# Kernel optimization log

Measured on AMD Instinct MI355X. Metric: run time of the kernel, lower is better.

## Reference

```python
import jax, jax.numpy as jnp
import numpy as np

D, H, L, FF, V, B, S = 512, 8, 6, 2048, 4096, 2, 4096
EPS = 1e-5

def _unit(v):
    return v / jnp.linalg.norm(v, axis=-1, keepdims=True)

def _unitelu(v):
    return jax.nn.elu(_unit(v))

def _ln(x, g, b):
    m = jnp.mean(x, axis=-1, keepdims=True)
    var = jnp.var(x, axis=-1, keepdims=True)
    return (x - m) * jax.lax.rsqrt(var + EPS) * g + b

def setup_inputs() -> dict:
    key = jax.random.key(0)
    ks = jax.random.split(key, 16)
    s = 0.02
    inp = {
        'input': jax.random.randint(ks[0], (B, S), 0, V),
        'emb': jax.random.normal(ks[1], (V, D)) * s,
        'Wq': jax.random.normal(ks[2], (L, D, D)) * s,
        'bq': jnp.zeros((L, D)),
        'Wk': jax.random.normal(ks[3], (L, D, D)) * s,
        'bk': jnp.zeros((L, D)),
        'Wv': jax.random.normal(ks[4], (L, D, D)) * s,
        'bv': jnp.zeros((L, D)),
        'Wo': jax.random.normal(ks[5], (L, D, D)) * s,
        'bo': jnp.zeros((L, D)),
        'W1': jax.random.normal(ks[6], (L, FF, D)) * s,
        'b1': jnp.zeros((L, FF)),
        'W2': jax.random.normal(ks[7], (L, D, FF)) * s,
        'b2': jnp.zeros((L, D)),
        'g2': jnp.ones((L, D)),
        'be2': jnp.zeros((L, D)),
        'Wfc': jax.random.normal(ks[8], (V, D)) * s,
        'bfc': jnp.zeros((V,)),
    }
    return inp

def reference(input, emb, Wq, bq, Wk, bk, Wv, bv, Wo, bo, W1, b1, W2, b2, g2, be2, Wfc, bfc):
    # h: [S, B, D] (seq-major, matching input.permute(1,0) then embedding)
    h = emb[input.T]
    for l in range(L):
        # linear kernelized attention: O(S * dh^2) per head, no SxS matrix
        k = _unitelu((h @ Wk[l].T + bk[l]).reshape(S, B, H, -1))  # [S,B,H,dh]
        v = (h @ Wv[l].T + bv[l]).reshape(S, B, H, -1)
        A = jnp.einsum('sbnq,sbnv->bnvq', k, v)                    # [B,H,dh,dh]
        q = _unit((h @ Wq[l].T + bq[l]).reshape(S, B, H, -1))
        o = jnp.einsum('sbnq,bnvq->sbnv', q, A).reshape(S, B, D)
        h = h + (o @ Wo[l].T + bo[l])
        f = jax.nn.relu(h @ W1[l].T + b1[l]) @ W2[l].T + b2[l]
        h = _ln(h + f, g2[l], be2[l])
    out = h @ Wfc.T + bfc          # [S, B, V]
    return out.transpose(1, 2, 0)  # [B, V, S]
```

## Files before the change

kernel.cpp:

```cpp
#include <hip/hip_runtime.h>
#include <hip/hip_bf16.h>

#define D_  512
#define H_  8
#define DH_ 64
#define L_  6
#define FF_ 2048
#define V_  4096
#define B_  2
#define S_  4096
#define SB_ (S_*B_)
#define DD_ ((size_t)D_*D_)
#define FD_ ((size_t)FF_*D_)
#define NTOT_ (4*DD_ + 2*FD_)
#define CVT_BLKS_ 20480

typedef unsigned short u16;
typedef unsigned int   u32;
typedef _Float16 f16;
typedef f16   f16x8 __attribute__((ext_vector_type(8)));
typedef float f32x4 __attribute__((ext_vector_type(4)));

__device__ __forceinline__ float us2f(u16 u){
  union { u32 i; float f; } c; c.i = ((u32)u) << 16; return c.f;
}
__device__ __forceinline__ u16 f2b(float f){
  union { float f; u32 i; } c; c.f = f;
  u32 x = c.i;
  x += 0x7FFF + ((x >> 16) & 1);
  return (u16)(x >> 16);
}
__device__ __forceinline__ float h2f(u16 u){
  union { u16 s; f16 h; } c; c.s = u; return (float)c.h;
}
__device__ __forceinline__ u16 f2h(float f){
  union { f16 h; u16 s; } c; c.h = (f16)f; return c.s;
}
__device__ __forceinline__ float ldf(const void* p, size_t i, int isbf){
  return isbf ? us2f(((const u16*)p)[i]) : ((const float*)p)[i];
}

typedef const __attribute__((address_space(1))) u32* gas_u32p;
typedef       __attribute__((address_space(3))) u32* las_u32p;
__device__ __forceinline__ void async16(const u16* g, u16* l){
  __builtin_amdgcn_global_load_lds((gas_u32p)(const void*)g, (las_u32p)(void*)l, 16, 0, 0);
}

__global__ __launch_bounds__(64) void detect_dtype(const void* emb, int* flag)
{
  const int t = threadIdx.x;
  u16 hw = ((const u16*)emb)[t];
  int e = (hw >> 7) & 0xFF;
  int ok = ((e > 96) && (e < 160)) || ((hw & 0x7FFF) == 0);
  unsigned long long m = __ballot(ok);
  if (t == 0) *flag = (__popcll(m) >= 56) ? 1 : 0;
}

__global__ __launch_bounds__(256) void prep_all(
    const void* Wq, const void* Wk, const void* Wv, const void* Wo,
    const void* W1, const void* W2, const void* Wfc,
    u16* __restrict__ dstAll, u16* __restrict__ dstFC,
    const int* __restrict__ inp, const void* emb,
    float* __restrict__ h, u16* __restrict__ hb, const int* flagp)
{
  const int isbf = *flagp;
  if (blockIdx.x >= CVT_BLKS_) {
    const int m = blockIdx.x - CVT_BLKS_;
    const int t = threadIdx.x;
    const int s = m >> 1, b = m & 1;
    const int tok = inp[b * S_ + s];
    #pragma unroll
    for (int hh = 0; hh < 2; hh++) {
      const int d = t + hh * 256;
      const float v = ldf(emb, (size_t)tok * D_ + d, isbf);
      h[(size_t)m * D_ + d] = v;
      hb[(size_t)m * D_ + d] = f2h(v);
    }
    return;
  }
  const size_t total6 = 6 * NTOT_;
  const size_t i = ((size_t)blockIdx.x * 256 + threadIdx.x) * 4;
  const void* src; size_t off; u16* dst;
  if (i < total6) {
    const int l = (int)(i / NTOT_);
    const size_t r = i - (size_t)l * NTOT_;
    const size_t n4 = 4 * DD_, nW1 = n4 + FD_;
    if (r < n4) {
      const int wsel = (int)(r / DD_);
      src = (wsel == 0) ? Wq : (wsel == 1) ? Wk : (wsel == 2) ? Wv : Wo;
      off = (size_t)l * DD_ + (r - (size_t)wsel * DD_);
    } else if (r < nW1) { src = W1; off = (size_t)l * FD_ + (r - n4); }
    else                { src = W2; off = (size_t)l * FD_ + (r - nW1); }
    dst = dstAll + i;
  } else {
    const size_t j = i - total6;
    if (j >= (size_t)V_ * D_) return;
    src = Wfc; off = j; dst = dstFC + j;
  }
  ushort4 o;
  if (isbf) {
    ushort4 u = *(const ushort4*)((const u16*)src + off);
    o = make_ushort4(f2h(us2f(u.x)), f2h(us2f(u.y)), f2h(us2f(u.z)), f2h(us2f(u.w)));
  } else {
    float4 f = *(const float4*)((const float*)src + off);
    o = make_ushort4(f2h(f.x), f2h(f.y), f2h(f.z), f2h(f.w));
  }
  *(ushort4*)dst = o;
}

template<int ACT, int OUTMODE, int PRE, int TPB, int LOG_TX, int LOG_TXZ>
__global__ __launch_bounds__(256) void gemm_pers(
    const u16* __restrict__ A, const u16* __restrict__ Bm,
    int bstride,
    const void* bias, size_t bias_off,
    u16* __restrict__ Cb, void* __restrict__ Cout,
    int M, int N, int K, const int* flagp)
{
  __shared__ u16 tile[(PRE + 1) * 8192];
  const int t = threadIdx.x, lane = t & 63, w = t >> 6;
  const int wr = w >> 1, wc = w & 1;
  const int col = lane & 15, quad = lane >> 4;
  const int srow = w * 16 + (lane >> 2);
  const int skol = (((lane & 3) ^ ((lane >> 3) & 3)) << 3);
  const int rswz = ((col >> 1) & 3);
  const int isbf = *flagp;
  const int vbase = blockIdx.x * TPB;

  float bpre3[(OUTMODE == 3) ? 16 : 1];
  float bpre0[(OUTMODE == 3) ? 1 : TPB][4];
  if (OUTMODE == 3) {
    const int by0 = vbase >> LOG_TXZ;
    #pragma unroll
    for (int i = 0; i < 4; i++)
      #pragma unroll
      for (int r = 0; r < 4; r++)
        bpre3[i * 4 + r] = ldf(bias, bias_off + (by0 << 7) + wr * 64 + i * 16 + quad * 4 + r, isbf);
  } else {
    #pragma unroll
    for (int g = 0; g < TPB; g++) {
      const int bxg = (vbase + g) & ((1 << LOG_TX) - 1);
      #pragma unroll
      for (int j = 0; j < 4; j++)
        bpre0[g][j] = ldf(bias, bias_off + (bxg << 7) + wc * 64 + j * 16 + col, isbf);
    }
  }

  int st = -1;
  const u16 *ag0 = nullptr, *ag1 = nullptr, *bg0 = nullptr, *bg1 = nullptr;
  auto set_tile = [&](int tp) {
    const int v  = vbase + tp;
    const int by = v >> LOG_TXZ;
    const int rr = v & ((1 << LOG_TXZ) - 1);
    const int bz = rr >> LOG_TX;
    const int bx = rr & ((1 << LOG_TX) - 1);
    ag0 = A + (size_t)((by << 7) + srow) * K + skol;
    ag1 = ag0 + (size_t)64 * K;
    bg0 = Bm + ((size_t)((bx << 7) + srow) * bstride + bz) * K + skol;
    bg1 = bg0 + (size_t)64 * bstride * K;
  };
  auto stage = [&](int u) {
    const int tp = u >> 4;
    if (tp != st) { st = tp; set_tile(tp); }
    const int k0 = (u & 15) << 5;
    const int bo = (u % (PRE + 1)) * 8192;
    async16(ag0 + k0, &tile[bo +        w * 512]);
    async16(ag1 + k0, &tile[bo + 2048 + w * 512]);
    async16(bg0 + k0, &tile[bo + 4096 + w * 512]);
    async16(bg1 + k0, &tile[bo + 6144 + w * 512]);
  };

  const int U = TPB * 16;
  #pragma unroll
  for (int p = 0; p < PRE; ++p) stage(p);
  if (PRE >= 2) asm volatile("s_waitcnt vmcnt(4)" ::: "memory");
  else          asm volatile("s_waitcnt vmcnt(0)" ::: "memory");
  __builtin_amdgcn_s_barrier();
  asm volatile("" ::: "memory");

  f32x4 acc[4][4] = {};
  for (int u = 0; u < U; ++u) {
    if (u + PRE < U) stage(u + PRE);
    const int cur = (u % (PRE + 1)) * 8192;
    f16x8 af[4], bf[4];
    #pragma unroll
    for (int i = 0; i < 4; i++)
      af[i] = *(const f16x8*)&tile[cur + (wr * 64 + i * 16 + col) * 32 + ((quad ^ rswz) * 8)];
    #pragma unroll
    for (int j = 0; j < 4; j++)
      bf[j] = *(const f16x8*)&tile[cur + 4096 + (wc * 64 + j * 16 + col) * 32 + ((quad ^ rswz) * 8)];
    #pragma unroll
    for (int i = 0; i < 4; i++)
      #pragma unroll
      for (int j = 0; j < 4; j++)
        acc[i][j] = __builtin_amdgcn_mfma_f32_16x16x32_f16(af[i], bf[j], acc[i][j], 0, 0, 0);

    if ((u & 15) == 15) {
      const int v  = vbase + (u >> 4);
      const int by = v >> LOG_TXZ;
      const int rr = v & ((1 << LOG_TXZ) - 1);
      const int bz = rr >> LOG_TX;
      const int bx = rr & ((1 << LOG_TX) - 1);
      const int bm = by << 7, bn = bx << 7;
      if (OUTMODE == 3) {
        const size_t obase = (size_t)bz * M * N;
        #pragma unroll
        for (int i = 0; i < 4; i++)
          #pragma unroll
          for (int r = 0; r < 4; r++) {
            const int m = bm + wr * 64 + i * 16 + quad * 4 + r;
            #pragma unroll
            for (int j = 0; j < 4; j++) {
              const int n = bn + wc * 64 + j * 16 + col;
              const float c = acc[i][j][r] + bpre3[i * 4 + r];
              const size_t oi = obase + (size_t)m * N + n;
              if (isbf) ((u16*)Cout)[oi] = f2b(c);
              else      ((float*)Cout)[oi] = c;
            }
          }
      } else {
        const int g = u >> 4;
        #pragma unroll
        for (int i = 0; i < 4; i++)
          #pragma unroll
          for (int r = 0; r < 4; r++) {
            const int m = bm + wr * 64 + i * 16 + quad * 4 + r;
            #pragma unroll
            for (int j = 0; j < 4; j++) {
              const int n = bn + wc * 64 + j * 16 + col;
              float c = acc[i][j][r] + bpre0[g][j];
              if (ACT == 1) c = fmaxf(c, 0.f);
              Cb[(size_t)m * N + n] = f2h(c);
            }
          }
      }
      const f32x4 z = {0.f, 0.f, 0.f, 0.f};
      #pragma unroll
      for (int i = 0; i < 4; i++)
        #pragma unroll
        for (int j = 0; j < 4; j++)
          acc[i][j] = z;
    }

    if (PRE >= 2 && u + 2 < U) asm volatile("s_waitcnt vmcnt(4)" ::: "memory");
    else                       asm volatile("s_waitcnt vmcnt(0)" ::: "memory");
    __builtin_amdgcn_s_barrier();
    asm volatile("" ::: "memory");
  }
}

__global__ __launch_bounds__(256) void gemm_qkv(
    const u16* __restrict__ A, const u16* __restrict__ Bm,
    const void* bq, const void* bk, const void* bv, size_t b_off,
    u16* __restrict__ qb, u16* __restrict__ kb, u16* __restrict__ vb,
    int K, const int* flagp)
{
  __shared__ u16 tile[3 * 8192];
  const int t = threadIdx.x, lane = t & 63, w = t >> 6;
  const int bm = blockIdx.y << 7, bn = blockIdx.x << 7;
  const int wr = w >> 1, wc = w & 1;
  const int col = lane & 15, quad = lane >> 4;

  const int srow = w * 16 + (lane >> 2);
  const int skol = (((lane & 3) ^ ((lane >> 3) & 3)) << 3);
  const u16* ag0 = A + (size_t)(bm + srow) * K + skol;
  const u16* ag1 = A + (size_t)(bm + 64 + srow) * K + skol;
  const u16* bg0 = Bm + (size_t)(bn + srow) * K + skol;
  const u16* bg1 = Bm + (size_t)(bn + 64 + srow) * K + skol;
  u16* la0 = &tile[       w * 512];
  u16* la1 = &tile[2048 + w * 512];
  u16* lb0 = &tile[4096 + w * 512];
  u16* lb1 = &tile[6144 + w * 512];

  const int nt = K >> 5;

  #pragma unroll
  for (int p = 0; p < 2; ++p) {
    const int k0 = p << 5, bo = p * 8192;
    async16(ag0 + k0, la0 + bo);
    async16(ag1 + k0, la1 + bo);
    async16(bg0 + k0, lb0 + bo);
    async16(bg1 + k0, lb1 + bo);
  }
  asm volatile("s_waitcnt vmcnt(4)" ::: "memory");
  __builtin_amdgcn_s_barrier();
  asm volatile("" ::: "memory");

  const int rswz = ((col >> 1) & 3);

  f32x4 acc[4][4] = {};
  for (int t2 = 0; t2 < nt; ++t2) {
    if (t2 + 2 < nt) {
      const int k0 = (t2 + 2) << 5;
      const int bo = ((t2 + 2) % 3) * 8192;
      async16(ag0 + k0, la0 + bo);
      async16(ag1 + k0, la1 + bo);
      async16(bg0 + k0, lb0 + bo);
      async16(bg1 + k0, lb1 + bo);
    }
    const int cur = (t2 % 3) * 8192;
    f16x8 af[4], bf[4];
    #pragma unroll
    for (int i = 0; i < 4; i++)
      af[i] = *(const f16x8*)&tile[cur + (wr * 64 + i * 16 + col) * 32 + ((quad ^ rswz) * 8)];
    #pragma unroll
    for (int j = 0; j < 4; j++)
      bf[j] = *(const f16x8*)&tile[cur + 4096 + (wc * 64 + j * 16 + col) * 32 + ((quad ^ rswz) * 8)];
    #pragma unroll
    for (int i = 0; i < 4; i++)
      #pragma unroll
      for (int j = 0; j < 4; j++)
        acc[i][j] = __builtin_amdgcn_mfma_f32_16x16x32_f16(af[i], bf[j], acc[i][j], 0, 0, 0);
    if (t2 + 2 < nt) asm volatile("s_waitcnt vmcnt(4)" ::: "memory");
    else             asm volatile("s_waitcnt vmcnt(0)" ::: "memory");
    __builtin_amdgcn_s_barrier();
    asm volatile("" ::: "memory");
  }

  const int isbf = *flagp;
  const int nbase = bn + wc * 64;
  const int sel = nbase >> 9;
  const int nl0 = nbase & 511;
  u16* outp = (sel == 0) ? qb : (sel == 1) ? kb : vb;
  const void* bias = (sel == 0) ? bq : (sel == 1) ? bk : bv;

  if (sel < 2) {
    #pragma unroll
    for (int i = 0; i < 4; i++) {
      #pragma unroll
      for (int r = 0; r < 4; r++) {
        float v[4]; float ss = 0.f;
        #pragma unroll
        for (int j = 0; j < 4; j++) {
          const int nl = nl0 + j * 16 + col;
          v[j] = acc[i][j][r] + ldf(bias, b_off + nl, isbf);
          ss += v[j] * v[j];
        }
        ss += __shfl_xor(ss, 1); ss += __shfl_xor(ss, 2);
        ss += __shfl_xor(ss, 4); ss += __shfl_xor(ss, 8);
        const float inv = rsqrtf(fmaxf(ss, 1e-30f));
        const int m = bm + wr * 64 + i * 16 + quad * 4 + r;
        #pragma unroll
        for (int j = 0; j < 4; j++) {
          float u = v[j] * inv;
          if (sel == 1) u = (u > 0.f) ? u : expm1f(u);
          outp[(size_t)m * 512 + nl0 + j * 16 + col] = f2h(u);
        }
      }
    }
  } else {
    #pragma unroll
    for (int i = 0; i < 4; i++)
      #pragma unroll
      for (int r = 0; r < 4; r++) {
        const int m = bm + wr * 64 + i * 16 + quad * 4 + r;
        #pragma unroll
        for (int j = 0; j < 4; j++) {
          const int nl = nl0 + j * 16 + col;
          outp[(size_t)m * 512 + nl] = f2h(acc[i][j][r] + ldf(bias, b_off + nl, isbf));
        }
      }
  }
}

template<int ACT, int OUTMODE, int PRE>
__global__ __launch_bounds__(256) void gemm_mfma64(
    const u16* __restrict__ A, const u16* __restrict__ Bm,
    const void* bias, size_t bias_off,
    const float* __restrict__ res,
    float* __restrict__ Cf, u16* __restrict__ Cb,
    int M, int N, int K, const int* flagp)
{
  __shared__ u16 tile[(PRE + 1) * 6144];
  const int t = threadIdx.x, lane = t & 63, w = t >> 6;
  const int bm = blockIdx.y << 6, bn = blockIdx.x << 7;
  const int wr = w >> 1, wc = w & 1;
  const int col = lane & 15, quad = lane >> 4;

  const int srow = w * 16 + (lane >> 2);
  const int skol = (((lane & 3) ^ ((lane >> 3) & 3)) << 3);
  const u16* ag  = A + (size_t)(bm + srow) * K + skol;
  const u16* bg0 = Bm + (size_t)(bn + srow) * K + skol;
  const u16* bg1 = Bm + (size_t)(bn + 64 + srow) * K + skol;
  u16* la  = &tile[       w * 512];
  u16* lb0 = &tile[2048 + w * 512];
  u16* lb1 = &tile[4096 + w * 512];

  const int nt = K >> 5;

  #pragma unroll
  for (int p = 0; p < PRE; ++p) {
    const int k0 = p << 5, bo = p * 6144;
    async16(ag  + k0, la  + bo);
    async16(bg0 + k0, lb0 + bo);
    async16(bg1 + k0, lb1 + bo);
  }
  if      (PRE >= 3) asm volatile("s_waitcnt vmcnt(6)" ::: "memory");
  else if (PRE == 2) asm volatile("s_waitcnt vmcnt(3)" ::: "memory");
  else               asm volatile("s_waitcnt vmcnt(0)" ::: "memory");
  __builtin_amdgcn_s_barrier();
  asm volatile("" ::: "memory");

  const int rswz = ((col >> 1) & 3);

  f32x4 acc[2][4] = {};
  for (int t2 = 0; t2 < nt; ++t2) {
    if (t2 + PRE < nt) {
      const int k0 = (t2 + PRE) << 5;
      const int bo = ((t2 + PRE) % (PRE + 1)) * 6144;
      async16(ag  + k0, la  + bo);
      async16(bg0 + k0, lb0 + bo);
      async16(bg1 + k0, lb1 + bo);
    }
    const int cur = (t2 % (PRE + 1)) * 6144;
    f16x8 af[2], bf[4];
    #pragma unroll
    for (int i = 0; i < 2; i++)
      af[i] = *(const f16x8*)&tile[cur + (wr * 32 + i * 16 + col) * 32 + ((quad ^ rswz) * 8)];
    #pragma unroll
    for (int j = 0; j < 4; j++)
      bf[j] = *(const f16x8*)&tile[cur + 2048 + (wc * 64 + j * 16 + col) * 32 + ((quad ^ rswz) * 8)];
    #pragma unroll
    for (int i = 0; i < 2; i++)
      #pragma unroll
      for (int j = 0; j < 4; j++)
        acc[i][j] = __builtin_amdgcn_mfma_f32_16x16x32_f16(af[i], bf[j], acc[i][j], 0, 0, 0);
    if (PRE >= 3) {
      if      (t2 + 3 < nt) asm volatile("s_waitcnt vmcnt(6)" ::: "memory");
      else if (t2 + 2 < nt) asm volatile("s_waitcnt vmcnt(3)" ::: "memory");
      else                  asm volatile("s_waitcnt vmcnt(0)" ::: "memory");
    } else if (PRE == 2) {
      if (t2 + 2 < nt) asm volatile("s_waitcnt vmcnt(3)" ::: "memory");
      else             asm volatile("s_waitcnt vmcnt(0)" ::: "memory");
    } else {
      asm volatile("s_waitcnt vmcnt(0)" ::: "memory");
    }
    __builtin_amdgcn_s_barrier();
    asm volatile("" ::: "memory");
  }

  const int isbf = *flagp;
  #pragma unroll
  for (int i = 0; i < 2; i++) {
    #pragma unroll
    for (int r = 0; r < 4; r++) {
      const int m = bm + wr * 32 + i * 16 + quad * 4 + r;
      #pragma unroll
      for (int j = 0; j < 4; j++) {
        const int n = bn + wc * 64 + j * 16 + col;
        float c = acc[i][j][r] + ldf(bias, bias_off + n, isbf);
        if (res) c += res[(size_t)m * N + n];
        if (ACT == 1) c = fmaxf(c, 0.f);
        if (OUTMODE == 0) {
          Cb[(size_t)m * N + n] = f2h(c);
        } else if (OUTMODE == 1) {
          Cf[(size_t)m * N + n] = c;
          Cb[(size_t)m * N + n] = f2h(c);
        } else {
          Cf[(size_t)m * N + n] = c;
        }
      }
    }
  }
}

#define KT_ 136
__global__ __launch_bounds__(256) void attn_acc_mfma(
    const u16* __restrict__ kbuf, const u16* __restrict__ vbuf,
    float* __restrict__ Apart)
{
  __shared__ u16 ktr[64 * KT_];
  __shared__ u16 vtr[64 * KT_];
  const int bh = blockIdx.x;
  const int b  = bh >> 3, n = bh & 7;
  const int s0 = blockIdx.y << 7;
  const int t = threadIdx.x, lane = t & 63, w = t >> 6;
  const int col = lane & 15, quad = lane >> 4;

  #pragma unroll
  for (int u = 0; u < 8; u++) {
    const int flat = u * 256 + t;
    const int row = flat >> 4, q4 = (flat & 15) << 2;
    const size_t g = ((size_t)(s0 + row) * B_ + b) * D_ + n * 64 + q4;
    ushort4 kk = *(const ushort4*)&kbuf[g];
    ushort4 vv = *(const ushort4*)&vbuf[g];
    ktr[(q4+0)*KT_ + row] = kk.x; ktr[(q4+1)*KT_ + row] = kk.y;
    ktr[(q4+2)*KT_ + row] = kk.z; ktr[(q4+3)*KT_ + row] = kk.w;
    vtr[(q4+0)*KT_ + row] = vv.x; vtr[(q4+1)*KT_ + row] = vv.y;
    vtr[(q4+2)*KT_ + row] = vv.z; vtr[(q4+3)*KT_ + row] = vv.w;
  }
  __syncthreads();

  f32x4 acc[4] = {};
  #pragma unroll
  for (int ks = 0; ks < 4; ks++) {
    const int k0 = ks * 32;
    f16x8 af = *(const f16x8*)&vtr[(w * 16 + col) * KT_ + k0 + quad * 8];
    #pragma unroll
    for (int j = 0; j < 4; j++) {
      f16x8 bf = *(const f16x8*)&ktr[(j * 16 + col) * KT_ + k0 + quad * 8];
      acc[j] = __builtin_amdgcn_mfma_f32_16x16x32_f16(af, bf, acc[j], 0, 0, 0);
    }
  }
  float* Ap = Apart + ((size_t)blockIdx.y * 16 + bh) * 4096;
  #pragma unroll
  for (int j = 0; j < 4; j++)
    #pragma unroll
    for (int r = 0; r < 4; r++) {
      const int vi = w * 16 + quad * 4 + r, qi = j * 16 + col;
      Ap[vi * 64 + qi] = acc[j][r];
    }
}

__global__ __launch_bounds__(256) void reduce_A(
    const float* __restrict__ Apart, u16* __restrict__ Ah)
{
  const int i = blockIdx.x * 256 + threadIdx.x;
  const int bh = i >> 12, idx = i & 4095;
  float s = 0.f;
  #pragma unroll
  for (int p = 0; p < 32; p++)
    s += Apart[((size_t)p * 16 + bh) * 4096 + idx];
  Ah[i] = f2h(s);
}

__global__ __launch_bounds__(256) void attn_apply_mfma(
    u16* __restrict__ qo, const u16* __restrict__ Ah)
{
  const int bh = blockIdx.x;
  const int b = bh >> 3, n = bh & 7;
  const int s0 = blockIdx.y << 7;
  const int t = threadIdx.x, lane = t & 63, w = t >> 6;
  const int col = lane & 15, quad = lane >> 4;

  const u16* Ab_ = Ah + (size_t)bh * 4096;
  f16x8 bf[4][2];
  #pragma unroll
  for (int j = 0; j < 4; j++)
    #pragma unroll
    for (int ks = 0; ks < 2; ks++)
      bf[j][ks] = *(const f16x8*)&Ab_[(j * 16 + col) * 64 + ks * 32 + quad * 8];

  const int srow_base = s0 + w * 32;
  f32x4 acc[2][4] = {};
  #pragma unroll
  for (int i = 0; i < 2; i++) {
    const int s = srow_base + i * 16 + col;
    const u16* qp = qo + ((size_t)s * B_ + b) * D_ + n * 64;
    f16x8 af0 = *(const f16x8*)&qp[quad * 8];
    f16x8 af1 = *(const f16x8*)&qp[32 + quad * 8];
    #pragma unroll
    for (int j = 0; j < 4; j++) {
      acc[i][j] = __builtin_amdgcn_mfma_f32_16x16x32_f16(af0, bf[j][0], acc[i][j], 0, 0, 0);
      acc[i][j] = __builtin_amdgcn_mfma_f32_16x16x32_f16(af1, bf[j][1], acc[i][j], 0, 0, 0);
    }
  }
  #pragma unroll
  for (int i = 0; i < 2; i++)
    #pragma unroll
    for (int r = 0; r < 4; r++) {
      const int s = srow_base + i * 16 + quad * 4 + r;
      u16* op = qo + ((size_t)s * B_ + b) * D_ + n * 64;
      #pragma unroll
      for (int j = 0; j < 4; j++)
        op[j * 16 + col] = f2h(acc[i][j][r]);
    }
}

__global__ __launch_bounds__(256) void ln_k(
    float* __restrict__ h, u16* __restrict__ hb,
    const void* g, size_t g_off, const void* be, size_t be_off, const int* flagp)
{
  const int isbf = *flagp;
  const int m = blockIdx.x, t = threadIdx.x;
  float* p = h + (size_t)m * D_;
  const float x0 = p[t], x1 = p[t + 256];
  __shared__ float red[4];
  float s = x0 + x1;
  #pragma unroll
  for (int off = 32; off >= 1; off >>= 1) s += __shfl_xor(s, off);
  if ((t & 63) == 0) red[t >> 6] = s;
  __syncthreads();
  const float mean = (red[0] + red[1] + red[2] + red[3]) * (1.f / 512.f);
  const float d0 = x0 - mean, d1 = x1 - mean;
  float s2 = d0 * d0 + d1 * d1;
  #pragma unroll
  for (int off = 32; off >= 1; off >>= 1) s2 += __shfl_xor(s2, off);
  __syncthreads();
  if ((t & 63) == 0) red[t >> 6] = s2;
  __syncthreads();
  const float var = (red[0] + red[1] + red[2] + red[3]) * (1.f / 512.f);
  const float sc = rsqrtf(var + 1e-5f);
  const float y0 = d0 * sc * ldf(g, g_off + t, isbf)       + ldf(be, be_off + t, isbf);
  const float y1 = d1 * sc * ldf(g, g_off + t + 256, isbf) + ldf(be, be_off + t + 256, isbf);
  p[t] = y0;       p[t + 256] = y1;
  hb[(size_t)m * D_ + t] = f2h(y0);
  hb[(size_t)m * D_ + t + 256] = f2h(y1);
}

extern "C" void kernel_launch(void* const* d_in, const int* in_sizes, int n_in,
                              void* d_out, int out_size, void* d_ws, size_t ws_size,
                              hipStream_t stream) {
  const int*  inp = (const int*) d_in[0];
  const void* emb = d_in[1];
  const void* Wq  = d_in[2];
  const void* bq  = d_in[3];
  const void* Wk  = d_in[4];
  const void* bk  = d_in[5];
  const void* Wv  = d_in[6];
  const void* bv  = d_in[7];
  const void* Wo  = d_in[8];
  const void* bo  = d_in[9];
  const void* W1  = d_in[10];
  const void* b1  = d_in[11];
  const void* W2  = d_in[12];
  const void* b2  = d_in[13];
  const void* g2  = d_in[14];
  const void* be2 = d_in[15];
  const void* Wfc = d_in[16];
  const void* bfc = d_in[17];

  char* ws = (char*)d_ws;
  float* h     = (float*)(ws);
  u16*   hb    = (u16*)  (ws + 16777216);
  u16*   qb    = (u16*)  (ws + 25165824);
  u16*   kb    = (u16*)  (ws + 33554432);
  u16*   vb    = (u16*)  (ws + 41943040);
  u16*   mid   = qb;
  float* Apart = (float*)(ws + 58720256);
  u16*   Ah16  = (u16*)  (ws + 67108864);
  u16*   WcAll = (u16*)  (ws + 67239936);
  u16*   WcFC  = (u16*)  (ws + 104988672);
  int*   flag  = (int*)  (ws + 109182976);

  detect_dtype<<<1, 64, 0, stream>>>(emb, flag);
  prep_all<<<CVT_BLKS_ + SB_, 256, 0, stream>>>(
      Wq, Wk, Wv, Wo, W1, W2, Wfc, WcAll, WcFC, inp, emb, h, hb, flag);

  const dim3 gQ64(D_ / 128, SB_ / 64);
  const dim3 gQKV(3 * D_ / 128, SB_ / 128);
  const dim3 gAT(B_ * H_, S_ / 128);

  for (int l = 0; l < L_; l++) {
    u16* Wcl = WcAll + (size_t)l * NTOT_;

    gemm_qkv<<<gQKV, 256, 0, stream>>>(hb, Wcl, bq, bk, bv, (size_t)l*D_, qb, kb, vb, D_, flag);

    attn_acc_mfma<<<gAT, 256, 0, stream>>>(kb, vb, Apart);
    reduce_A<<<256, 256, 0, stream>>>(Apart, Ah16);
    attn_apply_mfma<<<gAT, 256, 0, stream>>>(qb, Ah16);

    gemm_mfma64<0,1,3><<<gQ64, 256, 0, stream>>>(qb, Wcl + 3*DD_, bo, (size_t)l*D_, h, h, hb, SB_, D_, D_, flag);
    gemm_pers<1,0,2,2,4,4><<<512, 256, 0, stream>>>(hb, Wcl + 4*DD_, 1, b1, (size_t)l*FF_, mid, nullptr, SB_, FF_, D_, flag);
    gemm_mfma64<0,2,3><<<gQ64, 256, 0, stream>>>(mid, Wcl + 4*DD_ + FD_, b2, (size_t)l*D_, h, h, nullptr, SB_, D_, FF_, flag);
    ln_k<<<SB_, 256, 0, stream>>>(h, hb, g2, (size_t)l*D_, be2, (size_t)l*D_, flag);
  }

  gemm_pers<0,3,2,4,5,6><<<512, 256, 0, stream>>>(WcFC, hb, 2, bfc, 0, nullptr, d_out, V_, S_, D_, flag);
}
```

Measured before the change: 1.337 ms.

## Fold attention state into per-batch Wo weights, removing the attention-apply pass

```diff
diff --git a/kernel.cpp b/kernel.cpp
--- a/kernel.cpp
+++ b/kernel.cpp
@@ -463,6 +463,87 @@
   }
 }
 
+__global__ __launch_bounds__(256) void gemm_wo(
+    const u16* __restrict__ A,
+    const u16* __restrict__ Wp,
+    const void* bias, size_t bias_off,
+    float* __restrict__ h, u16* __restrict__ hb, const int* flagp)
+{
+  __shared__ u16 tile[4 * 6144];
+  const int t = threadIdx.x, lane = t & 63, w = t >> 6;
+  const int bm = blockIdx.y << 6, bn = blockIdx.x << 7, bz = blockIdx.z;
+  const int wr = w >> 1, wc = w & 1;
+  const int col = lane & 15, quad = lane >> 4;
+
+  const int srow = w * 16 + (lane >> 2);
+  const int skol = (((lane & 3) ^ ((lane >> 3) & 3)) << 3);
+  const u16* ag  = A + ((size_t)(bm + srow) * 2 + bz) * 512 + skol;
+  const u16* bg0 = Wp + (size_t)bz * 512 * 512 + (size_t)(bn + srow) * 512 + skol;
+  const u16* bg1 = bg0 + (size_t)64 * 512;
+  u16* la  = &tile[       w * 512];
+  u16* lb0 = &tile[2048 + w * 512];
+  u16* lb1 = &tile[4096 + w * 512];
+
+  #pragma unroll
+  for (int p = 0; p < 3; ++p) {
+    const int k0 = p << 5, bo = p * 6144;
+    async16(ag  + k0, la  + bo);
+    async16(bg0 + k0, lb0 + bo);
+    async16(bg1 + k0, lb1 + bo);
+  }
+  asm volatile("s_waitcnt vmcnt(6)" ::: "memory");
+  __builtin_amdgcn_s_barrier();
+  asm volatile("" ::: "memory");
+
+  const int rswz = ((col >> 1) & 3);
+
+  f32x4 acc[2][4] = {};
+  for (int t2 = 0; t2 < 16; ++t2) {
+    if (t2 + 3 < 16) {
+      const int k0 = (t2 + 3) << 5;
+      const int bo = ((t2 + 3) & 3) * 6144;
+      async16(ag  + k0, la  + bo);
+      async16(bg0 + k0, lb0 + bo);
+      async16(bg1 + k0, lb1 + bo);
+    }
+    const int cur = (t2 & 3) * 6144;
+    f16x8 af[2], bf[4];
+    #pragma unroll
+    for (int i = 0; i < 2; i++)
+      af[i] = *(const f16x8*)&tile[cur + (wr * 32 + i * 16 + col) * 32 + ((quad ^ rswz) * 8)];
+    #pragma unroll
+    for (int j = 0; j < 4; j++)
+      bf[j] = *(const f16x8*)&tile[cur + 2048 + (wc * 64 + j * 16 + col) * 32 + ((quad ^ rswz) * 8)];
+    #pragma unroll
+    for (int i = 0; i < 2; i++)
+      #pragma unroll
+      for (int j = 0; j < 4; j++)
+        acc[i][j] = __builtin_amdgcn_mfma_f32_16x16x32_f16(af[i], bf[j], acc[i][j], 0, 0, 0);
+    if      (t2 + 3 < 16) asm volatile("s_waitcnt vmcnt(6)" ::: "memory");
+    else if (t2 + 2 < 16) asm volatile("s_waitcnt vmcnt(3)" ::: "memory");
+    else                  asm volatile("s_waitcnt vmcnt(0)" ::: "memory");
+    __builtin_amdgcn_s_barrier();
+    asm volatile("" ::: "memory");
+  }
+
+  const int isbf = *flagp;
+  #pragma unroll
+  for (int i = 0; i < 2; i++) {
+    #pragma unroll
+    for (int r = 0; r < 4; r++) {
+      const size_t g = (size_t)(bm + wr * 32 + i * 16 + quad * 4 + r) * 2 + bz;
+      #pragma unroll
+      for (int j = 0; j < 4; j++) {
+        const int n = bn + wc * 64 + j * 16 + col;
+        float c = acc[i][j][r] + ldf(bias, bias_off + n, isbf);
+        c += h[g * 512 + n];
+        h[g * 512 + n] = c;
+        hb[g * 512 + n] = f2h(c);
+      }
+    }
+  }
+}
+
 #define KT_ 136
 __global__ __launch_bounds__(256) void attn_acc_mfma(
     const u16* __restrict__ kbuf, const u16* __restrict__ vbuf,
@@ -511,58 +592,58 @@
     }
 }
 
-__global__ __launch_bounds__(256) void reduce_A(
-    const float* __restrict__ Apart, u16* __restrict__ Ah)
-{
-  const int i = blockIdx.x * 256 + threadIdx.x;
-  const int bh = i >> 12, idx = i & 4095;
-  float s = 0.f;
-  #pragma unroll
-  for (int p = 0; p < 32; p++)
-    s += Apart[((size_t)p * 16 + bh) * 4096 + idx];
-  Ah[i] = f2h(s);
-}
-
-__global__ __launch_bounds__(256) void attn_apply_mfma(
-    u16* __restrict__ qo, const u16* __restrict__ Ah)
-{
+#define WPT_ 72
+__global__ __launch_bounds__(256) void form_wp(
+    const float* __restrict__ Apart, const u16* __restrict__ Wo16,
+    u16* __restrict__ wp)
+{
+  __shared__ u16 aT[64 * WPT_];
   const int bh = blockIdx.x;
-  const int b = bh >> 3, n = bh & 7;
-  const int s0 = blockIdx.y << 7;
+  const int b = bh >> 3, hh = bh & 7;
   const int t = threadIdx.x, lane = t & 63, w = t >> 6;
   const int col = lane & 15, quad = lane >> 4;
 
-  const u16* Ab_ = Ah + (size_t)bh * 4096;
-  f16x8 bf[4][2];
-  #pragma unroll
-  for (int j = 0; j < 4; j++)
-    #pragma unroll
-    for (int ks = 0; ks < 2; ks++)
-      bf[j][ks] = *(const f16x8*)&Ab_[(j * 16 + col) * 64 + ks * 32 + quad * 8];
-
-  const int srow_base = s0 + w * 32;
-  f32x4 acc[2][4] = {};
-  #pragma unroll
-  for (int i = 0; i < 2; i++) {
-    const int s = srow_base + i * 16 + col;
-    const u16* qp = qo + ((size_t)s * B_ + b) * D_ + n * 64;
-    f16x8 af0 = *(const f16x8*)&qp[quad * 8];
-    f16x8 af1 = *(const f16x8*)&qp[32 + quad * 8];
-    #pragma unroll
-    for (int j = 0; j < 4; j++) {
-      acc[i][j] = __builtin_amdgcn_mfma_f32_16x16x32_f16(af0, bf[j][0], acc[i][j], 0, 0, 0);
-      acc[i][j] = __builtin_amdgcn_mfma_f32_16x16x32_f16(af1, bf[j][1], acc[i][j], 0, 0, 0);
-    }
-  }
-  #pragma unroll
-  for (int i = 0; i < 2; i++)
+  #pragma unroll
+  for (int e = 0; e < 4; e++) {
+    const int idx = t * 16 + e * 4;
+    float4 s = make_float4(0.f, 0.f, 0.f, 0.f);
+    for (int p = 0; p < 32; p++) {
+      const float4 v = *(const float4*)&Apart[((size_t)p * 16 + bh) * 4096 + idx];
+      s.x += v.x; s.y += v.y; s.z += v.z; s.w += v.w;
+    }
+    const int vi = idx >> 6, qi = idx & 63;
+    aT[(qi + 0) * WPT_ + vi] = f2h(s.x);
+    aT[(qi + 1) * WPT_ + vi] = f2h(s.y);
+    aT[(qi + 2) * WPT_ + vi] = f2h(s.z);
+    aT[(qi + 3) * WPT_ + vi] = f2h(s.w);
+  }
+  __syncthreads();
+
+  f32x4 acc[8][4] = {};
+  #pragma unroll
+  for (int ks = 0; ks < 2; ks++) {
+    f16x8 bf[4];
+    #pragma unroll
+    for (int j = 0; j < 4; j++)
+      bf[j] = *(const f16x8*)&aT[(j * 16 + col) * WPT_ + ks * 32 + quad * 8];
+    #pragma unroll
+    for (int i = 0; i < 8; i++) {
+      const int out = w * 128 + i * 16 + col;
+      f16x8 af = *(const f16x8*)&Wo16[(size_t)out * 512 + hh * 64 + ks * 32 + quad * 8];
+      #pragma unroll
+      for (int j = 0; j < 4; j++)
+        acc[i][j] = __builtin_amdgcn_mfma_f32_16x16x32_f16(af, bf[j], acc[i][j], 0, 0, 0);
+    }
+  }
+  u16* wpb = wp + (size_t)b * 512 * 512;
+  #pragma unroll
+  for (int i = 0; i < 8; i++)
     #pragma unroll
     for (int r = 0; r < 4; r++) {
-      const int s = srow_base + i * 16 + quad * 4 + r;
-      u16* op = qo + ((size_t)s * B_ + b) * D_ + n * 64;
+      const int out = w * 128 + i * 16 + quad * 4 + r;
       #pragma unroll
       for (int j = 0; j < 4; j++)
-        op[j * 16 + col] = f2h(acc[i][j][r]);
+        wpb[(size_t)out * 512 + hh * 64 + j * 16 + col] = f2h(acc[i][j][r]);
     }
 }
 
@@ -625,9 +706,9 @@
   u16*   qb    = (u16*)  (ws + 25165824);
   u16*   kb    = (u16*)  (ws + 33554432);
   u16*   vb    = (u16*)  (ws + 41943040);
+  u16*   wp    = vb;
   u16*   mid   = qb;
   float* Apart = (float*)(ws + 58720256);
-  u16*   Ah16  = (u16*)  (ws + 67108864);
   u16*   WcAll = (u16*)  (ws + 67239936);
   u16*   WcFC  = (u16*)  (ws + 104988672);
   int*   flag  = (int*)  (ws + 109182976);
@@ -637,6 +718,7 @@
       Wq, Wk, Wv, Wo, W1, W2, Wfc, WcAll, WcFC, inp, emb, h, hb, flag);
 
   const dim3 gQ64(D_ / 128, SB_ / 64);
+  const dim3 gWO(D_ / 128, S_ / 64, 2);
   const dim3 gQKV(3 * D_ / 128, SB_ / 128);
   const dim3 gAT(B_ * H_, S_ / 128);
 
@@ -646,14 +728,13 @@
     gemm_qkv<<<gQKV, 256, 0, stream>>>(hb, Wcl, bq, bk, bv, (size_t)l*D_, qb, kb, vb, D_, flag);
 
     attn_acc_mfma<<<gAT, 256, 0, stream>>>(kb, vb, Apart);
-    reduce_A<<<256, 256, 0, stream>>>(Apart, Ah16);
-    attn_apply_mfma<<<gAT, 256, 0, stream>>>(qb, Ah16);
-
-    gemm_mfma64<0,1,3><<<gQ64, 256, 0, stream>>>(qb, Wcl + 3*DD_, bo, (size_t)l*D_, h, h, hb, SB_, D_, D_, flag);
+    form_wp<<<B_ * H_, 256, 0, stream>>>(Apart, Wcl + 3*DD_, wp);
+    gemm_wo<<<gWO, 256, 0, stream>>>(qb, wp, bo, (size_t)l*D_, h, hb, flag);
+
     gemm_pers<1,0,2,2,4,4><<<512, 256, 0, stream>>>(hb, Wcl + 4*DD_, 1, b1, (size_t)l*FF_, mid, nullptr, SB_, FF_, D_, flag);
     gemm_mfma64<0,2,3><<<gQ64, 256, 0, stream>>>(mid, Wcl + 4*DD_ + FD_, b2, (size_t)l*D_, h, h, nullptr, SB_, D_, FF_, flag);
     ln_k<<<SB_, 256, 0, stream>>>(h, hb, g2, (size_t)l*D_, be2, (size_t)l*D_, flag);
   }
 
-  gemm_pers<0,3,2,4,5,6><<<512, 256, 0, stream>>>(WcFC, hb, 2, bfc, 0, nullptr, d_out, V_, S_, D_, flag);
-}
+  gemm_pers<0,3,2,2,5,6><<<1024, 256, 0, stream>>>(WcFC, hb, 2, bfc, 0, nullptr, d_out, V_, S_, D_, flag);
+}
```

Measured after the change: 1.348 ms. Within noise of the previous version (+0.8%).
